# Kernel tuning notes

Measured on AMD Instinct MI355X. Metric: run time of the kernel, lower is better.

Reference implementation:

```python
import jax, jax.numpy as jnp
import numpy as np

CLAMP_LO, CLAMP_HI = 1e-4, 1.0 - 1e-4
EPS = 1e-8

def setup_inputs() -> dict:
    key = jax.random.key(0)
    k1, k2 = jax.random.split(key)
    B, T, C = 32, 2048, 512
    x = jax.random.normal(k1, (B, T, C), dtype=jnp.float32)
    # init_alpha = 0.9 -> logit(0.9) = log(9), repeated per channel (plus tiny jitter)
    init = jnp.float32(np.log(0.9 / 0.1))
    logit_alpha = init + 0.01 * jax.random.normal(k2, (C,), dtype=jnp.float32)
    return {"x": x, "logit_alpha": logit_alpha}

def reference(x, logit_alpha):
    B, T, C = x.shape
    dt = x.dtype
    a = jnp.clip(jax.nn.sigmoid(logit_alpha), CLAMP_LO, CLAMP_HI).astype(dt)  # [C]
    t = jnp.arange(T, dtype=dt)[:, None]                                      # [T,1]
    a_pow = a[None, :] ** t                                                   # [T,C]
    divisor = jnp.maximum(a_pow, EPS)                                         # [T,C]
    scale = jnp.concatenate(
        [jnp.ones((1, C), dtype=dt), jnp.broadcast_to((1.0 - a)[None, :], (T - 1, C))],
        axis=0,
    )                                                                         # [T,C]
    w = (a_pow * scale)[None]                                                 # [1,T,C]
    y = jnp.cumsum(x * w, axis=1) / divisor[None]                             # [B,T,C]
    return y
```

## Files before the change

kernel.cpp:

```cpp
#include <hip/hip_runtime.h>
#include <math.h>


#define B_ 32
#define T_ 2048
#define C_ 512
#define WAVES 16
#define TCHUNK (T_ / WAVES)
#define CPB 64

__global__ __launch_bounds__(WAVES * 64, 1)
void ema_scan_kernel(const float* __restrict__ x,
                     const float* __restrict__ logit_alpha,
                     float* __restrict__ y) {
    __shared__ float csum[WAVES][CPB];

    const int tid  = threadIdx.x;
    const int wave = tid >> 6;
    const int lane = tid & 63;
    const int b    = blockIdx.x >> 3;
    const int cg   = blockIdx.x & 7;
    const int c    = (cg << 6) + lane;

    const float z = logit_alpha[c];
    float a = 1.0f / (1.0f + expf(-z));
    a = fminf(fmaxf(a, 1e-4f), 1.0f - 1e-4f);
    const float oma = 1.0f - a;

    const int t0 = wave * TCHUNK;
    const float l2a = log2f(a);
    const float ap0 = exp2f((float)t0 * l2a);

    const float* __restrict__ xp = x + ((size_t)b * T_ + t0) * C_ + c;
    float* __restrict__ yp       = y + ((size_t)b * T_ + t0) * C_ + c;

    if (wave < WAVES - 1) {
        float ap = ap0;
        float s  = 0.0f;
        #pragma unroll 8
        for (int i = 0; i < TCHUNK; ++i) {
            float w = (t0 + i == 0) ? 1.0f : ap * oma;
            s = fmaf(xp[(size_t)i * C_], w, s);
            ap *= a;
        }
        csum[wave][lane] = s;
    }
    __syncthreads();

    float S = 0.0f;
    for (int w2 = 0; w2 < wave; ++w2) S += csum[w2][lane];

    float ap    = ap0;
    const float inva = 1.0f / a;
    float invap = exp2f(-(float)t0 * l2a);
    #pragma unroll 8
    for (int i = 0; i < TCHUNK; ++i) {
        float w = (t0 + i == 0) ? 1.0f : ap * oma;
        S = fmaf(xp[(size_t)i * C_], w, S);
        const float invd = fminf(invap, 1e8f);
        yp[(size_t)i * C_] = S * invd;
        ap    *= a;
        invap *= inva;
    }
}

extern "C" void kernel_launch(void* const* d_in, const int* in_sizes, int n_in,
                              void* d_out, int out_size, void* d_ws, size_t ws_size,
                              hipStream_t stream) {
    const float* x  = (const float*)d_in[0];
    const float* la = (const float*)d_in[1];
    float* y = (float*)d_out;

    dim3 grid(B_ * (C_ / CPB));
    dim3 block(WAVES * 64);
    hipLaunchKernelGGL(ema_scan_kernel, grid, block, 0, stream, x, la, y);
}
```

Before: 251.6 us.

## Split EMA scan into two kernels with global chunk partials and float4 access

```diff
diff --git a/kernel.cpp b/kernel.cpp
--- a/kernel.cpp
+++ b/kernel.cpp
@@ -5,62 +5,116 @@
 #define B_ 32
 #define T_ 2048
 #define C_ 512
-#define WAVES 16
-#define TCHUNK (T_ / WAVES)
-#define CPB 64
+#define TB 64
+#define NTB (T_ / TB)
 
-__global__ __launch_bounds__(WAVES * 64, 1)
-void ema_scan_kernel(const float* __restrict__ x,
-                     const float* __restrict__ logit_alpha,
-                     float* __restrict__ y) {
-    __shared__ float csum[WAVES][CPB];
+typedef float f32x4 __attribute__((ext_vector_type(4)));
 
-    const int tid  = threadIdx.x;
-    const int wave = tid >> 6;
-    const int lane = tid & 63;
-    const int b    = blockIdx.x >> 3;
-    const int cg   = blockIdx.x & 7;
-    const int c    = (cg << 6) + lane;
+__device__ __forceinline__ float clamp_sig(float z) {
+    float a = 1.0f / (1.0f + expf(-z));
+    return fminf(fmaxf(a, 1e-4f), 1.0f - 1e-4f);
+}
 
-    const float z = logit_alpha[c];
-    float a = 1.0f / (1.0f + expf(-z));
-    a = fminf(fmaxf(a, 1e-4f), 1.0f - 1e-4f);
-    const float oma = 1.0f - a;
+__global__ __launch_bounds__(256, 2)
+void ema_partials(const float* __restrict__ x,
+                  const float* __restrict__ la,
+                  float* __restrict__ ws) {
+    const int tid = threadIdx.x;
+    const int wv = tid >> 6, ln = tid & 63;
+    const int b  = blockIdx.x >> 4;
+    const int pr = blockIdx.x & 15;
+    const int tb = (pr << 1) | (wv >> 1);
+    const int c0 = ((wv & 1) << 8) | (ln << 2);
+    const int t0 = tb * TB;
 
-    const int t0 = wave * TCHUNK;
-    const float l2a = log2f(a);
-    const float ap0 = exp2f((float)t0 * l2a);
+    const float4 z4 = *(const float4*)(la + c0);
+    float a[4], oma[4], ap[4];
+    const float zz[4] = {z4.x, z4.y, z4.z, z4.w};
+    #pragma unroll
+    for (int j = 0; j < 4; ++j) {
+        a[j]   = clamp_sig(zz[j]);
+        oma[j] = 1.0f - a[j];
+        ap[j]  = exp2f((float)t0 * log2f(a[j]));
+    }
 
-    const float* __restrict__ xp = x + ((size_t)b * T_ + t0) * C_ + c;
-    float* __restrict__ yp       = y + ((size_t)b * T_ + t0) * C_ + c;
+    const float4* __restrict__ xp =
+        (const float4*)(x + ((size_t)b * T_ + t0) * C_ + c0);
+    float s[4] = {0.f, 0.f, 0.f, 0.f};
+    #pragma unroll 8
+    for (int i = 0; i < TB; ++i) {
+        const float4 xv = xp[(size_t)i * (C_ >> 2)];
+        const bool z0 = (t0 + i) == 0;
+        float w0 = z0 ? 1.0f : ap[0] * oma[0];
+        float w1 = z0 ? 1.0f : ap[1] * oma[1];
+        float w2 = z0 ? 1.0f : ap[2] * oma[2];
+        float w3 = z0 ? 1.0f : ap[3] * oma[3];
+        s[0] = fmaf(xv.x, w0, s[0]);
+        s[1] = fmaf(xv.y, w1, s[1]);
+        s[2] = fmaf(xv.z, w2, s[2]);
+        s[3] = fmaf(xv.w, w3, s[3]);
+        #pragma unroll
+        for (int j = 0; j < 4; ++j) ap[j] *= a[j];
+    }
+    *(float4*)(ws + (size_t)(b * NTB + tb) * C_ + c0) =
+        make_float4(s[0], s[1], s[2], s[3]);
+}
 
-    if (wave < WAVES - 1) {
-        float ap = ap0;
-        float s  = 0.0f;
-        #pragma unroll 8
-        for (int i = 0; i < TCHUNK; ++i) {
-            float w = (t0 + i == 0) ? 1.0f : ap * oma;
-            s = fmaf(xp[(size_t)i * C_], w, s);
-            ap *= a;
-        }
-        csum[wave][lane] = s;
+__global__ __launch_bounds__(256, 2)
+void ema_apply(const float* __restrict__ x,
+               const float* __restrict__ la,
+               const float* __restrict__ ws,
+               float* __restrict__ y) {
+    const int tid = threadIdx.x;
+    const int wv = tid >> 6, ln = tid & 63;
+    const int b  = blockIdx.x >> 4;
+    const int pr = blockIdx.x & 15;
+    const int tb = (pr << 1) | (wv >> 1);
+    const int c0 = ((wv & 1) << 8) | (ln << 2);
+    const int t0 = tb * TB;
+
+    const float4 z4 = *(const float4*)(la + c0);
+    float a[4], oma[4], ap[4], inva[4], invap[4];
+    const float zz[4] = {z4.x, z4.y, z4.z, z4.w};
+    #pragma unroll
+    for (int j = 0; j < 4; ++j) {
+        a[j]     = clamp_sig(zz[j]);
+        oma[j]   = 1.0f - a[j];
+        const float l2a = log2f(a[j]);
+        ap[j]    = exp2f((float)t0 * l2a);
+        invap[j] = exp2f(-(float)t0 * l2a);
+        inva[j]  = 1.0f / a[j];
     }
-    __syncthreads();
 
-    float S = 0.0f;
-    for (int w2 = 0; w2 < wave; ++w2) S += csum[w2][lane];
+    float S[4] = {0.f, 0.f, 0.f, 0.f};
+    for (int q = 0; q < tb; ++q) {
+        const float4 p = *(const float4*)(ws + (size_t)(b * NTB + q) * C_ + c0);
+        S[0] += p.x; S[1] += p.y; S[2] += p.z; S[3] += p.w;
+    }
 
-    float ap    = ap0;
-    const float inva = 1.0f / a;
-    float invap = exp2f(-(float)t0 * l2a);
-    #pragma unroll 8
-    for (int i = 0; i < TCHUNK; ++i) {
-        float w = (t0 + i == 0) ? 1.0f : ap * oma;
-        S = fmaf(xp[(size_t)i * C_], w, S);
-        const float invd = fminf(invap, 1e8f);
-        yp[(size_t)i * C_] = S * invd;
-        ap    *= a;
-        invap *= inva;
+    const float4* __restrict__ xp =
+        (const float4*)(x + ((size_t)b * T_ + t0) * C_ + c0);
+    float* __restrict__ yp = y + ((size_t)b * T_ + t0) * C_ + c0;
+
+    #pragma unroll 4
+    for (int i = 0; i < TB; ++i) {
+        const float4 xv = xp[(size_t)i * (C_ >> 2)];
+        const bool z0 = (t0 + i) == 0;
+        float w0 = z0 ? 1.0f : ap[0] * oma[0];
+        float w1 = z0 ? 1.0f : ap[1] * oma[1];
+        float w2 = z0 ? 1.0f : ap[2] * oma[2];
+        float w3 = z0 ? 1.0f : ap[3] * oma[3];
+        S[0] = fmaf(xv.x, w0, S[0]);
+        S[1] = fmaf(xv.y, w1, S[1]);
+        S[2] = fmaf(xv.z, w2, S[2]);
+        S[3] = fmaf(xv.w, w3, S[3]);
+        f32x4 out;
+        out.x = S[0] * fminf(invap[0], 1e8f);
+        out.y = S[1] * fminf(invap[1], 1e8f);
+        out.z = S[2] * fminf(invap[2], 1e8f);
+        out.w = S[3] * fminf(invap[3], 1e8f);
+        __builtin_nontemporal_store(out, (f32x4*)(yp + (size_t)i * C_));
+        #pragma unroll
+        for (int j = 0; j < 4; ++j) { ap[j] *= a[j]; invap[j] *= inva[j]; }
     }
 }
 
@@ -69,9 +123,11 @@
                               hipStream_t stream) {
     const float* x  = (const float*)d_in[0];
     const float* la = (const float*)d_in[1];
-    float* y = (float*)d_out;
+    float* y  = (float*)d_out;
+    float* ws = (float*)d_ws;
 
-    dim3 grid(B_ * (C_ / CPB));
-    dim3 block(WAVES * 64);
-    hipLaunchKernelGGL(ema_scan_kernel, grid, block, 0, stream, x, la, y);
+    dim3 grid(B_ * (NTB / 2));
+    dim3 block(256);
+    hipLaunchKernelGGL(ema_partials, grid, block, 0, stream, x, la, ws);
+    hipLaunchKernelGGL(ema_apply,    grid, block, 0, stream, x, la, ws, y);
 }
```

Measured after the change: 253.0 us. No clear change (+0.5%).
